# Optimization experiments

Measured on AMD Instinct MI355X. Metric: run time of the kernel, lower is better.

The kernel has to match this reference:

```python
import jax, jax.numpy as jnp
from jax import lax
import numpy as np

VOCAB = 50000
E = 301  # 300-dim pretrained + appended ones column
D = 25
NUM_CLASSES = 5


def setup_inputs() -> dict:
    key = jax.random.key(0)
    ks = jax.random.split(key, 8)
    B, S = 2048, 128
    words = jax.random.randint(ks[0], (B, S), 0, VOCAB)
    emb = jax.random.normal(ks[1], (VOCAB, E - 1), dtype=jnp.float32)
    # hstack ones column as in __init__
    emb_table = jnp.concatenate([emb, jnp.ones((VOCAB, 1), jnp.float32)], axis=1)
    A = jax.random.normal(ks[2], (D, E, D), dtype=jnp.float32) * 0.02
    W = jax.random.normal(ks[3], (E, D), dtype=jnp.float32) * 0.02
    V = jax.random.normal(ks[4], (D, D), dtype=jnp.float32) * 0.02
    b = jax.random.normal(ks[5], (D,), dtype=jnp.float32) * 0.02
    out_W = jax.random.normal(ks[6], (NUM_CLASSES, D), dtype=jnp.float32) * 0.02
    out_b = jax.random.normal(ks[7], (NUM_CLASSES,), dtype=jnp.float32) * 0.02
    return {"words": words, "batch_size": B, "emb_table": emb_table,
            "A": A, "W": W, "V": V, "b": b, "out_W": out_W, "out_b": out_b}


def reference(words, batch_size, emb_table, A, W, V, b, out_W, out_b):
    x_seq = emb_table[words]                      # [B, S, E] frozen embedding gather
    h0 = jnp.zeros((batch_size, D), jnp.float32).at[:, -1].set(1.0)

    def step(h, x):  # x: [B, E], h: [B, D]
        # a[b,i] = sum_{e,j} x[b,e] A[i,e,j] h[b,j]  (bilinear tensor term)
        a = jnp.einsum('be,ied,bd->bi', x, A, h)
        lin = x @ W + h @ V + b
        return jnp.tanh(a + lin), None

    h, _ = lax.scan(step, h0, jnp.swapaxes(x_seq, 0, 1))  # scan over S
    logits = h @ out_W.T + out_b                 # [B, num_classes]
    return jax.nn.sigmoid(logits)
```

## Files before the change

kernel.cpp:

```cpp
#include <hip/hip_runtime.h>
#include <math.h>

#define VOCAB 50000
#define EE 301
#define DD 25
#define SEQ 128
#define NC 5
#define BROW 768
#define NUSE 700
#define TROW 704

__global__ __launch_bounds__(256) void build_B(
    const float* __restrict__ A, const float* __restrict__ W,
    float* __restrict__ Bmat)
{
    int e = blockIdx.x;
    for (int c = threadIdx.x; c < BROW; c += 256) {
        float v = 0.f;
        if (c < NUSE) {
            int i = c / 28, j = c % 28;
            if (j < 25)       v = A[((size_t)i * EE + e) * DD + j];
            else if (j == 25) v = W[(size_t)e * DD + i];
        }
        Bmat[(size_t)e * BROW + c] = v;
    }
}

__global__ __launch_bounds__(256, 2) void gemm_T(
    const float* __restrict__ emb,
    const float* __restrict__ Bmat,
    float* __restrict__ T)
{
    __shared__ float As[16][132];
    __shared__ float Bs[16][132];
    int tid = threadIdx.x;
    int tx = tid & 15, ty = tid >> 4;
    int m0 = blockIdx.x * 128;
    int n0 = blockIdx.y * 128;

    float acc[8][8];
#pragma unroll
    for (int a = 0; a < 8; ++a)
#pragma unroll
        for (int c = 0; c < 8; ++c) acc[a][c] = 0.f;

    for (int k0 = 0; k0 < EE; k0 += 16) {
#pragma unroll
        for (int it = 0; it < 8; ++it) {
            int ml = ty + 16 * it;
            int m = m0 + ml, k = k0 + tx;
            As[tx][ml] = (m < VOCAB && k < EE) ? emb[(size_t)m * EE + k] : 0.f;
        }
#pragma unroll
        for (int it = 0; it < 2; ++it) {
            int idx = tid + it * 256;
            int kl = idx >> 5, nl = (idx & 31) * 4;
            int k = k0 + kl;
            float4 v = make_float4(0.f, 0.f, 0.f, 0.f);
            if (k < EE)
                v = *(const float4*)(Bmat + (size_t)k * BROW + n0 + nl);
            *(float4*)(&Bs[kl][nl]) = v;
        }
        __syncthreads();
#pragma unroll
        for (int kk = 0; kk < 16; ++kk) {
            float4 a0 = *(const float4*)&As[kk][ty * 4];
            float4 a1 = *(const float4*)&As[kk][64 + ty * 4];
            float4 b0 = *(const float4*)&Bs[kk][tx * 4];
            float4 b1 = *(const float4*)&Bs[kk][64 + tx * 4];
            float av[8] = {a0.x, a0.y, a0.z, a0.w, a1.x, a1.y, a1.z, a1.w};
            float bv[8] = {b0.x, b0.y, b0.z, b0.w, b1.x, b1.y, b1.z, b1.w};
#pragma unroll
            for (int a = 0; a < 8; ++a)
#pragma unroll
                for (int c = 0; c < 8; ++c)
                    acc[a][c] = fmaf(av[a], bv[c], acc[a][c]);
        }
        __syncthreads();
    }

#pragma unroll
    for (int gi = 0; gi < 2; ++gi) {
#pragma unroll
        for (int r = 0; r < 4; ++r) {
            int m = m0 + gi * 64 + ty * 4 + r;
            if (m < VOCAB) {
                float* row = T + (size_t)m * TROW;
#pragma unroll
                for (int gc = 0; gc < 2; ++gc) {
                    int n = n0 + gc * 64 + tx * 4;
                    if (n < TROW) {
                        int a = gi * 4 + r, c = gc * 4;
                        *(float4*)(row + n) = make_float4(
                            acc[a][c], acc[a][c + 1], acc[a][c + 2], acc[a][c + 3]);
                    }
                }
            }
        }
    }
}

__global__ __launch_bounds__(256) void rnn_scan_np4(
    const int*   __restrict__ words,
    const float* __restrict__ T,
    const float* __restrict__ V,
    const float* __restrict__ bvec,
    const float* __restrict__ outW,
    const float* __restrict__ outB,
    float* __restrict__ out,
    int B)
{
    int tid = threadIdx.x;
    int g = tid >> 5, i = tid & 31;
    int b = blockIdx.x * 8 + g;
    bool act = (i < DD) && (b < B);
    int ii = (i < DD) ? i : (DD - 1);
    int bsafe = (b < B) ? b : 0;
    const int* wr = words + (size_t)bsafe * SEQ;

    float Vcol[DD];
#pragma unroll
    for (int j = 0; j < DD; ++j) Vcol[j] = V[j * DD + ii];
    float bi = bvec[ii];

    float hr[DD];
#pragma unroll
    for (int j = 0; j < DD; ++j) hr[j] = 0.f;
    hr[DD - 1] = 1.f;

    bool sse = ((b & 3) == 0) && ((i & 3) == 0);
    const float* base = T + (size_t)ii * 28;

    float4 cur[7], nxt[7];
    {
        const float* R = base + (size_t)wr[0] * TROW;
#pragma unroll
        for (int u = 0; u < 7; ++u) cur[u] = *(const float4*)(R + u * 4);
    }

    float hnew = 0.f;
    for (int t = 0; t < SEQ; ++t) {
        int wn = wr[(t + 1 < SEQ) ? t + 1 : t];
        const float* Rn = base + (size_t)wn * TROW;
#pragma unroll
        for (int u = 0; u < 7; ++u) nxt[u] = *(const float4*)(Rn + u * 4);

        float Tj[28];
#pragma unroll
        for (int u = 0; u < 7; ++u) {
            Tj[u * 4 + 0] = cur[u].x; Tj[u * 4 + 1] = cur[u].y;
            Tj[u * 4 + 2] = cur[u].z; Tj[u * 4 + 3] = cur[u].w;
        }
        float qv = Tj[25];

        float a;
        if (sse) {
            float p0 = 0.f, p1 = 0.f, p2 = 0.f, p3 = 0.f;
#pragma unroll
            for (int j = 0; j < 24; j += 4) {
                p0 = __fadd_rn(p0, __fmul_rn(Tj[j],     hr[j]));
                p1 = __fadd_rn(p1, __fmul_rn(Tj[j + 1], hr[j + 1]));
                p2 = __fadd_rn(p2, __fmul_rn(Tj[j + 2], hr[j + 2]));
                p3 = __fadd_rn(p3, __fmul_rn(Tj[j + 3], hr[j + 3]));
            }
            float s02 = __fadd_rn(p0, p2);
            float s13 = __fadd_rn(p1, p3);
            a = __fadd_rn(s02, s13);
            a = __fadd_rn(a, __fmul_rn(Tj[24], hr[24]));
        } else {
            a = 0.f;
#pragma unroll
            for (int j = 0; j < DD; ++j)
                a = __fadd_rn(a, __fmul_rn(Tj[j], hr[j]));
        }

        float r2 = 0.f;
#pragma unroll
        for (int j = 0; j < DD; ++j)
            r2 = fmaf(hr[j], Vcol[j], r2);

        float lin = __fadd_rn(__fadd_rn(qv, r2), bi);
        float pre = __fadd_rn(a, lin);
        hnew = act ? (float)tanh((double)pre) : 0.f;

#pragma unroll
        for (int j = 0; j < DD; ++j)
            hr[j] = __shfl(hnew, j, 32);

#pragma unroll
        for (int u = 0; u < 7; ++u) cur[u] = nxt[u];
    }

    if (i < NC && b < B) {
        float acc = 0.f;
#pragma unroll
        for (int j = 0; j < DD; ++j)
            acc = fmaf(hr[j], outW[i * DD + j], acc);
        float l = __fadd_rn(acc, outB[i]);
        out[(size_t)b * NC + i] = (float)(1.0 / (1.0 + exp(-(double)l)));
    }
}

extern "C" void kernel_launch(void* const* d_in, const int* in_sizes, int n_in,
                              void* d_out, int out_size, void* d_ws, size_t ws_size,
                              hipStream_t stream)
{
    const int*   words = (const int*)d_in[0];
    const float* emb   = (const float*)d_in[2];
    const float* A     = (const float*)d_in[3];
    const float* W     = (const float*)d_in[4];
    const float* V     = (const float*)d_in[5];
    const float* bias  = (const float*)d_in[6];
    const float* outW  = (const float*)d_in[7];
    const float* outB  = (const float*)d_in[8];
    float* out = (float*)d_out;
    int B = in_sizes[0] / SEQ;

    float* Bmat = (float*)d_ws;
    float* T    = (float*)((char*)d_ws + (1 << 20));

    build_B<<<EE, 256, 0, stream>>>(A, W, Bmat);
    gemm_T<<<dim3((VOCAB + 127) / 128, 6), 256, 0, stream>>>(emb, Bmat, T);
    rnn_scan_np4<<<(B + 7) / 8, 256, 0, stream>>>(words, T, V, bias, outW, outB, out, B);
}
```

Before: 584.1 us.

## Double-buffer shared-memory tiles in gemm_T with register prefetch

Converts the embedding-by-B GEMM to double-buffered shared memory. The next K-tile is prefetched into registers while the current tile is computed, then stored to the alternate buffer, so only one barrier is needed per iteration. The aim is to hide global-load latency behind the FMA loop. In exchange it doubles LDS use and adds register pressure on top of the 8x8 accumulators, which could reduce occupancy under launch_bounds(256,2).

```diff
diff --git a/kernel.cpp b/kernel.cpp
--- a/kernel.cpp
+++ b/kernel.cpp
@@ -31,8 +31,8 @@
     const float* __restrict__ Bmat,
     float* __restrict__ T)
 {
-    __shared__ float As[16][132];
-    __shared__ float Bs[16][132];
+    __shared__ float As[2][16][132];
+    __shared__ float Bs[2][16][132];
     int tid = threadIdx.x;
     int tx = tid & 15, ty = tid >> 4;
     int m0 = blockIdx.x * 128;
@@ -44,30 +44,50 @@
 #pragma unroll
         for (int c = 0; c < 8; ++c) acc[a][c] = 0.f;
 
+    float  ar[8];
+    float4 br[2];
+    int kl0 = tid >> 5, nl0 = (tid & 31) * 4;
+
+#pragma unroll
+    for (int it = 0; it < 8; ++it) {
+        int m = m0 + ty + 16 * it, k = tx;
+        ar[it] = (m < VOCAB && k < EE) ? emb[(size_t)m * EE + k] : 0.f;
+    }
+#pragma unroll
+    for (int it = 0; it < 2; ++it) {
+        int k = kl0 + 8 * it;
+        br[it] = (k < EE) ? *(const float4*)(Bmat + (size_t)k * BROW + n0 + nl0)
+                          : make_float4(0.f, 0.f, 0.f, 0.f);
+    }
+#pragma unroll
+    for (int it = 0; it < 8; ++it) As[0][tx][ty + 16 * it] = ar[it];
+#pragma unroll
+    for (int it = 0; it < 2; ++it) *(float4*)(&Bs[0][kl0 + 8 * it][nl0]) = br[it];
+    __syncthreads();
+
+    int buf = 0;
     for (int k0 = 0; k0 < EE; k0 += 16) {
-#pragma unroll
-        for (int it = 0; it < 8; ++it) {
-            int ml = ty + 16 * it;
-            int m = m0 + ml, k = k0 + tx;
-            As[tx][ml] = (m < VOCAB && k < EE) ? emb[(size_t)m * EE + k] : 0.f;
-        }
-#pragma unroll
-        for (int it = 0; it < 2; ++it) {
-            int idx = tid + it * 256;
-            int kl = idx >> 5, nl = (idx & 31) * 4;
-            int k = k0 + kl;
-            float4 v = make_float4(0.f, 0.f, 0.f, 0.f);
-            if (k < EE)
-                v = *(const float4*)(Bmat + (size_t)k * BROW + n0 + nl);
-            *(float4*)(&Bs[kl][nl]) = v;
-        }
-        __syncthreads();
+        int k1 = k0 + 16;
+        bool more = (k1 < EE);
+        if (more) {
+#pragma unroll
+            for (int it = 0; it < 8; ++it) {
+                int m = m0 + ty + 16 * it, k = k1 + tx;
+                ar[it] = (m < VOCAB && k < EE) ? emb[(size_t)m * EE + k] : 0.f;
+            }
+#pragma unroll
+            for (int it = 0; it < 2; ++it) {
+                int k = k1 + kl0 + 8 * it;
+                br[it] = (k < EE) ? *(const float4*)(Bmat + (size_t)k * BROW + n0 + nl0)
+                                  : make_float4(0.f, 0.f, 0.f, 0.f);
+            }
+        }
 #pragma unroll
         for (int kk = 0; kk < 16; ++kk) {
-            float4 a0 = *(const float4*)&As[kk][ty * 4];
-            float4 a1 = *(const float4*)&As[kk][64 + ty * 4];
-            float4 b0 = *(const float4*)&Bs[kk][tx * 4];
-            float4 b1 = *(const float4*)&Bs[kk][64 + tx * 4];
+            float4 a0 = *(const float4*)&As[buf][kk][ty * 4];
+            float4 a1 = *(const float4*)&As[buf][kk][64 + ty * 4];
+            float4 b0 = *(const float4*)&Bs[buf][kk][tx * 4];
+            float4 b1 = *(const float4*)&Bs[buf][kk][64 + tx * 4];
             float av[8] = {a0.x, a0.y, a0.z, a0.w, a1.x, a1.y, a1.z, a1.w};
             float bv[8] = {b0.x, b0.y, b0.z, b0.w, b1.x, b1.y, b1.z, b1.w};
 #pragma unroll
@@ -76,7 +96,15 @@
                 for (int c = 0; c < 8; ++c)
                     acc[a][c] = fmaf(av[a], bv[c], acc[a][c]);
         }
-        __syncthreads();
+        if (more) {
+            int nb = buf ^ 1;
+#pragma unroll
+            for (int it = 0; it < 8; ++it) As[nb][tx][ty + 16 * it] = ar[it];
+#pragma unroll
+            for (int it = 0; it < 2; ++it) *(float4*)(&Bs[nb][kl0 + 8 * it][nl0]) = br[it];
+            __syncthreads();
+            buf = nb;
+        }
     }
 
 #pragma unroll
```

New measurement: 512.0 us. 1.14x faster.
